# Kernel tuning notes

Measured on AMD Instinct MI355X. Metric: run time of the kernel, lower is better.

## Reference

```python
import jax, jax.numpy as jnp
import numpy as np

N_NODES, N_EDGES, NODE_D, EDGE_D, EMB_D, N_GRAPHS = 50000, 800000, 128, 100, 92, 256
N_CONV, FC_D, N_FC, CUTOFF = 3, 128, 2, 6.0


def setup_inputs() -> dict:
    key = jax.random.key(0)
    ks = jax.random.split(key, 24)
    s = 0.05
    inp = {
        "z": jax.random.randint(ks[0], (N_NODES,), 0, 100, dtype=jnp.int32),
        "R": jax.random.normal(ks[1], (N_NODES, 3), dtype=jnp.float32) * 5.0,
        "edge_index": jax.random.randint(ks[2], (2, N_EDGES), 0, N_NODES, dtype=jnp.int32),
        "batch": jnp.sort(jax.random.randint(ks[3], (N_NODES,), 0, N_GRAPHS, dtype=jnp.int32)),
        # learned parameters
        "embedding": jax.random.uniform(ks[4], (100, EMB_D), dtype=jnp.float32),
        "emb_w": jax.random.normal(ks[5], (EMB_D, NODE_D), dtype=jnp.float32) * s,
        "emb_b": jnp.zeros((NODE_D,), jnp.float32),
        "conv_w": jax.random.normal(ks[6], (N_CONV, 2 * NODE_D + EDGE_D, 2 * NODE_D), dtype=jnp.float32) * s,
        "conv_b": jnp.zeros((N_CONV, 2 * NODE_D), jnp.float32),
        "ln_g": jnp.ones((N_CONV, NODE_D), jnp.float32),
        "ln_b": jnp.zeros((N_CONV, NODE_D), jnp.float32),
        "cfc_w": jax.random.normal(ks[7], (NODE_D, FC_D), dtype=jnp.float32) * s,
        "cfc_b": jnp.zeros((FC_D,), jnp.float32),
        "fc_w": jax.random.normal(ks[8], (N_FC, FC_D, FC_D), dtype=jnp.float32) * s,
        "fc_b": jnp.zeros((N_FC, FC_D), jnp.float32),
        "out_w": jax.random.normal(ks[9], (FC_D, 1), dtype=jnp.float32) * s,
        "out_b": jnp.zeros((1,), jnp.float32),
    }
    return inp


def _gaussian_smearing(d):
    offsets = jnp.linspace(0.0, CUTOFF, EDGE_D, dtype=d.dtype)  # [EDGE_D]
    coeff = -0.5 / (offsets[1] - offsets[0]) ** 2
    return jnp.exp(coeff * (d[:, None] - offsets[None, :]) ** 2)  # [E, EDGE_D]


def _layernorm(x, g, b, eps=1e-5):
    mu = x.mean(-1, keepdims=True)
    var = x.var(-1, keepdims=True)
    return (x - mu) / jnp.sqrt(var + eps) * g + b


def reference(z, R, edge_index, batch, embedding, emb_w, emb_b, conv_w, conv_b,
              ln_g, ln_b, cfc_w, cfc_b, fc_w, fc_b, out_w, out_b):
    src, dst = edge_index[0], edge_index[1]  # messages flow src(j) -> dst(i)
    d = jnp.linalg.norm(R[src] - R[dst], axis=-1)  # [E]
    edge_attr = _gaussian_smearing(d)  # [E, EDGE_D]

    x = embedding[z] @ emb_w + emb_b  # [N, NODE_D]
    n = x.shape[0]
    for l in range(conv_w.shape[0]):
        xi, xj = x[dst], x[src]  # gather [E, NODE_D]
        zc = jnp.concatenate([xi, xj, edge_attr], axis=1) @ conv_w[l] + conv_b[l]  # [E, 2*NODE_D]
        z1, z2 = jnp.split(zc, 2, axis=1)
        msg = jax.nn.sigmoid(z1) * jax.nn.softplus(z2)  # [E, NODE_D]
        agg = jax.ops.segment_sum(msg, dst, num_segments=n)  # scatter-add
        x = jax.nn.softplus(_layernorm(agg, ln_g[l], ln_b[l]) + x)

    # global mean pool over graphs
    sums = jax.ops.segment_sum(x, batch, num_segments=N_GRAPHS)
    cnts = jax.ops.segment_sum(jnp.ones((n, 1), x.dtype), batch, num_segments=N_GRAPHS)
    mol = sums / jnp.maximum(cnts, 1.0)  # [N_GRAPHS, NODE_D]

    h = jax.nn.softplus(mol @ cfc_w + cfc_b)
    for l in range(fc_w.shape[0]):
        h = jax.nn.softplus(h @ fc_w[l] + fc_b[l])
    return h @ out_w + out_b  # energy [N_GRAPHS, 1]
```

## Files before the change

### kernel.cpp

```cpp
#include <hip/hip_runtime.h>
#include <hip/hip_bf16.h>
#include <cmath>

#define N_NODES 50000
#define N_EDGES 800000
#define NODE_DIM 128
#define EDGE_DIM 100
#define EMB_DIM 92
#define N_GRAPHS 256

typedef __attribute__((ext_vector_type(8))) short short8_t;
typedef __attribute__((ext_vector_type(4))) float float4_t;

__device__ __forceinline__ float softplus_f(float v) {
    return v > 20.0f ? v : __logf(1.0f + __expf(v));
}
__device__ __forceinline__ float sigmoid_f(float v) {
    return 1.0f / (1.0f + __expf(-v));
}

__global__ void deg_kernel(const int* __restrict__ ei, int* __restrict__ deg) {
    int e = blockIdx.x * blockDim.x + threadIdx.x;
    if (e >= N_EDGES) return;
    atomicAdd(&deg[ei[N_EDGES + e]], 1);
}

#define SB 1024
__global__ void scan1_kernel(const int* __restrict__ deg, int* __restrict__ rp,
                             int* __restrict__ bsum) {
    __shared__ int buf[SB];
    int b = blockIdx.x, t = threadIdx.x, i = b * SB + t;
    int v = (i < N_NODES) ? deg[i] : 0;
    buf[t] = v;
    __syncthreads();
    for (int off = 1; off < SB; off <<= 1) {
        int a = (t >= off) ? buf[t - off] : 0;
        __syncthreads();
        buf[t] += a;
        __syncthreads();
    }
    if (i < N_NODES) rp[i] = buf[t] - v;
    if (t == SB - 1) bsum[b] = buf[t];
}
__global__ void scan2_kernel(int* __restrict__ bsum, int n) {
    if (threadIdx.x == 0) {
        int s = 0;
        for (int i = 0; i < n; i++) { int v = bsum[i]; bsum[i] = s; s += v; }
    }
}
__global__ void scan3_kernel(int* __restrict__ rp, const int* __restrict__ bsum) {
    int i = blockIdx.x * SB + threadIdx.x;
    if (i < N_NODES) rp[i] += bsum[blockIdx.x];
    if (i == 0) rp[N_NODES] = N_EDGES;
}

__global__ void fill_kernel(const int* __restrict__ ei, const float* __restrict__ R,
                            const int* __restrict__ row_ptr, int* __restrict__ cnt2,
                            int* __restrict__ s_src, float* __restrict__ s_d) {
    int e = blockIdx.x * blockDim.x + threadIdx.x;
    if (e >= N_EDGES) return;
    int s = ei[e];
    int dst = ei[N_EDGES + e];
    float dx = R[3 * s + 0] - R[3 * dst + 0];
    float dy = R[3 * s + 1] - R[3 * dst + 1];
    float dz = R[3 * s + 2] - R[3 * dst + 2];
    float d = sqrtf(dx * dx + dy * dy + dz * dz);
    int pos = row_ptr[dst] + atomicAdd(&cnt2[dst], 1);
    s_src[pos] = s;
    s_d[pos] = d;
}

__global__ void gb_kernel(const int* __restrict__ batch, int* __restrict__ gs) {
    int i = blockIdx.x * 256 + threadIdx.x;
    if (i > N_NODES) return;
    int b = (i < N_NODES) ? batch[i] : N_GRAPHS;
    int pb = (i == 0) ? -1 : batch[i - 1];
    for (int g = pb + 1; g <= b; g++) gs[g] = i;
}

__global__ void wcvt_kernel(const float* __restrict__ conv_w, __hip_bfloat16* __restrict__ Webf) {
    int i = blockIdx.x * 256 + threadIdx.x;
    if (i >= 3 * EDGE_DIM * 256) return;
    int l = i / (EDGE_DIM * 256), r = i - l * (EDGE_DIM * 256);
    Webf[i] = (__hip_bfloat16)conv_w[(size_t)l * 356 * 256 + 256 * 256 + r];
}

__global__ void wprep_kernel(const float* __restrict__ conv_w, short* __restrict__ WbB) {
    int idx = blockIdx.x * 256 + threadIdx.x;
    if (idx >= 3 * 4 * 32 * 64 * 8) return;
    int j = idx & 7;
    int lane = (idx >> 3) & 63;
    int nt = (idx >> 9) & 31;
    int kc = (idx >> 14) & 3;
    int l = idx >> 16;
    int k = kc * 32 + (lane >> 4) * 8 + j;
    int nl = lane & 15;
    int row, col;
    if (nt < 16) { row = k; col = nt * 16 + nl; }
    else { row = 128 + k; col = (nt - 16) * 16 + nl; }
    __hip_bfloat16 bv = (__hip_bfloat16)conv_w[(size_t)l * 356 * 256 + (size_t)row * 256 + col];
    WbB[idx] = *(short*)&bv;
}

__global__ void embed_kernel(const int* __restrict__ z, const float* __restrict__ emb,
                             const float* __restrict__ emb_w, const float* __restrict__ emb_b,
                             float* __restrict__ x, __hip_bfloat16* __restrict__ xb) {
    __shared__ float er[EMB_DIM * 8];
    __shared__ int zi[8];
    int base = blockIdx.x * 8;
    int t = threadIdx.x;
    if (t < 8) zi[t] = z[base + t];
    __syncthreads();
    for (int idx = t; idx < EMB_DIM * 8; idx += 128) {
        int k = idx >> 3, j = idx & 7;
        er[idx] = emb[zi[j] * EMB_DIM + k];
    }
    __syncthreads();
    float acc[8];
    float bb = emb_b[t];
#pragma unroll
    for (int j = 0; j < 8; j++) acc[j] = bb;
    for (int k = 0; k < EMB_DIM; k++) {
        float w = emb_w[k * NODE_DIM + t];
        float4 ja = *(const float4*)&er[k * 8];
        float4 jb = *(const float4*)&er[k * 8 + 4];
        acc[0] = fmaf(w, ja.x, acc[0]); acc[1] = fmaf(w, ja.y, acc[1]);
        acc[2] = fmaf(w, ja.z, acc[2]); acc[3] = fmaf(w, ja.w, acc[3]);
        acc[4] = fmaf(w, jb.x, acc[4]); acc[5] = fmaf(w, jb.y, acc[5]);
        acc[6] = fmaf(w, jb.z, acc[6]); acc[7] = fmaf(w, jb.w, acc[7]);
    }
#pragma unroll
    for (int j = 0; j < 8; j++) {
        x[(base + j) * NODE_DIM + t] = acc[j];
        xb[(base + j) * NODE_DIM + t] = (__hip_bfloat16)acc[j];
    }
}

__global__ __launch_bounds__(256) void node_mfma_kernel(
    const __hip_bfloat16* __restrict__ xb, const short* __restrict__ WbB,
    const float* __restrict__ bl, float* __restrict__ P1, float* __restrict__ P2) {
    int t = threadIdx.x;
    int wv = t >> 6, lane = t & 63;
    int mrow = lane & 15, q = lane >> 4;
    int base = blockIdx.x * 16;
    const short* xr = (const short*)xb + (size_t)(base + mrow) * 128 + q * 8;
    float4_t acc[8];
#pragma unroll
    for (int i = 0; i < 8; i++) acc[i] = (float4_t){0.f, 0.f, 0.f, 0.f};
#pragma unroll
    for (int kc = 0; kc < 4; kc++) {
        short8_t a = *(const short8_t*)(xr + kc * 32);
#pragma unroll
        for (int i = 0; i < 8; i++) {
            int nt = wv * 8 + i;
            short8_t b = *(const short8_t*)&WbB[((size_t)(kc * 32 + nt) * 64 + lane) * 8];
            acc[i] = __builtin_amdgcn_mfma_f32_16x16x32_bf16(a, b, acc[i], 0, 0, 0);
        }
    }
#pragma unroll
    for (int i = 0; i < 8; i++) {
        int nt = wv * 8 + i;
        int np = nt * 16 + mrow;
        if (np < 256) {
            float bb = bl[np];
#pragma unroll
            for (int r = 0; r < 4; r++)
                P1[(size_t)(base + q * 4 + r) * 256 + np] = acc[i][r] + bb;
        } else {
#pragma unroll
            for (int r = 0; r < 4; r++)
                P2[(size_t)(base + q * 4 + r) * 256 + (np - 256)] = acc[i][r];
        }
    }
}

#define NTAP 10
__global__ __launch_bounds__(256) void node_edge_kernel(
    const int* __restrict__ row_ptr, const int* __restrict__ s_src,
    const float* __restrict__ s_d, const float* __restrict__ P1,
    const float* __restrict__ P2, const __hip_bfloat16* __restrict__ We,
    float* __restrict__ agg) {
    const float sp_ = 6.0f / 99.0f;
    const float inv_s = 99.0f / 6.0f;
    const float coeff = -0.5f * inv_s * inv_s;
    int node = blockIdx.x * 2 + (threadIdx.x >> 7);
    int c = threadIdx.x & 127;
    int e0 = row_ptr[node], e1 = row_ptr[node + 1];
    float a1 = P1[(size_t)node * 256 + c];
    float a2 = P1[(size_t)node * 256 + 128 + c];
    float acc = 0.f;
    float dvA = 0.f, b1A = 0.f, b2A = 0.f;
    int srcB = 0; float dvB = 0.f;
    if (e0 < e1) {
        int s0 = s_src[e0];
        dvA = s_d[e0];
        b1A = P2[(size_t)s0 * 256 + c];
        b2A = P2[(size_t)s0 * 256 + 128 + c];
    }
    if (e0 + 1 < e1) { srcB = s_src[e0 + 1]; dvB = s_d[e0 + 1]; }
    for (int e = e0; e < e1; e++) {
        float b1 = b1A, b2 = b2A, dv = dvA;
        if (e + 1 < e1) {
            b1A = P2[(size_t)srcB * 256 + c];
            b2A = P2[(size_t)srcB * 256 + 128 + c];
            dvA = dvB;
        }
        if (e + 2 < e1) { srcB = s_src[e + 2]; dvB = s_d[e + 2]; }
        float z1 = a1 + b1, z2 = a2 + b2;
        if (dv <= 6.34f) {
            int k0 = max(0, min(EDGE_DIM - NTAP, (int)ceilf(dv * inv_s - 4.5f)));
            const __hip_bfloat16* wr = We + k0 * 256 + c;
#pragma unroll
            for (int i = 0; i < NTAP; i++) {
                float df = dv - (float)(k0 + i) * sp_;
                float ee = __expf(coeff * df * df);
                z1 = fmaf((float)wr[i * 256], ee, z1);
                z2 = fmaf((float)wr[i * 256 + 128], ee, z2);
            }
        }
        acc += sigmoid_f(z1) * softplus_f(z2);
    }
    agg[(size_t)node * 128 + c] = acc;
}

__global__ void ln_kernel(const float* __restrict__ agg, const float* __restrict__ g,
                          const float* __restrict__ b, float* __restrict__ x,
                          __hip_bfloat16* __restrict__ xb) {
    __shared__ float sm[4][2];
    int t = threadIdx.x;
    int r = blockIdx.x * 2 + (t >> 7);
    int c = t & 127;
    float a = agg[(size_t)r * 128 + c];
    float s1 = a, s2 = a * a;
#pragma unroll
    for (int off = 32; off > 0; off >>= 1) {
        s1 += __shfl_xor(s1, off);
        s2 += __shfl_xor(s2, off);
    }
    int wv = t >> 6;
    if ((t & 63) == 0) { sm[wv][0] = s1; sm[wv][1] = s2; }
    __syncthreads();
    int w0 = (t >> 7) * 2;
    float S1 = sm[w0][0] + sm[w0 + 1][0];
    float S2 = sm[w0][1] + sm[w0 + 1][1];
    float mu = S1 * (1.0f / 128.0f);
    float var = S2 * (1.0f / 128.0f) - mu * mu;
    float rstd = rsqrtf(fmaxf(var, 0.f) + 1e-5f);
    float xv = x[(size_t)r * 128 + c];
    float res = softplus_f((a - mu) * rstd * g[c] + b[c] + xv);
    x[(size_t)r * 128 + c] = res;
    xb[(size_t)r * 128 + c] = (__hip_bfloat16)res;
}

__global__ void pool_head_kernel(const float* __restrict__ x, const int* __restrict__ gs,
                                 const float* __restrict__ cfc_w, const float* __restrict__ cfc_b,
                                 const float* __restrict__ fc_w, const float* __restrict__ fc_b,
                                 const float* __restrict__ out_w, const float* __restrict__ out_b,
                                 float* __restrict__ out) {
    int g = blockIdx.x, c = threadIdx.x;
    int n0 = gs[g], n1 = gs[g + 1];
    float s = 0.f;
    for (int n = n0; n < n1; n++) s += x[(size_t)n * 128 + c];
    __shared__ float h[128], h2[128];
    h[c] = s / fmaxf((float)(n1 - n0), 1.0f);
    __syncthreads();
    float acc = cfc_b[c];
    for (int k = 0; k < 128; k++) acc = fmaf(h[k], cfc_w[k * 128 + c], acc);
    h2[c] = softplus_f(acc);
    __syncthreads();
    for (int l = 0; l < 2; l++) {
        const float* W = fc_w + l * 128 * 128;
        acc = fc_b[l * 128 + c];
        for (int k = 0; k < 128; k++) acc = fmaf(h2[k], W[k * 128 + c], acc);
        __syncthreads();
        h2[c] = softplus_f(acc);
        __syncthreads();
    }
    h[c] = h2[c] * out_w[c];
    __syncthreads();
    for (int off = 64; off > 0; off >>= 1) {
        if (c < off) h[c] += h[c + off];
        __syncthreads();
    }
    if (c == 0) out[g] = h[0] + out_b[0];
}

extern "C" void kernel_launch(void* const* d_in, const int* in_sizes, int n_in,
                              void* d_out, int out_size, void* d_ws, size_t ws_size,
                              hipStream_t stream) {
    const int*   z      = (const int*)d_in[0];
    const float* R      = (const float*)d_in[1];
    const int*   ei     = (const int*)d_in[2];
    const int*   batch  = (const int*)d_in[3];
    const float* emb    = (const float*)d_in[4];
    const float* emb_w  = (const float*)d_in[5];
    const float* emb_b  = (const float*)d_in[6];
    const float* conv_w = (const float*)d_in[7];
    const float* conv_b = (const float*)d_in[8];
    const float* ln_g   = (const float*)d_in[9];
    const float* ln_b   = (const float*)d_in[10];
    const float* cfc_w  = (const float*)d_in[11];
    const float* cfc_b  = (const float*)d_in[12];
    const float* fc_w   = (const float*)d_in[13];
    const float* fc_b   = (const float*)d_in[14];
    const float* out_w  = (const float*)d_in[15];
    const float* out_b  = (const float*)d_in[16];
    float* out = (float*)d_out;

    float* ws    = (float*)d_ws;
    float* x     = ws;
    float* agg   = x + 6400000;
    float* P1    = agg + 6400000;
    float* P2    = P1 + 12800000;
    float* s_d   = P2 + 12800000;
    int* s_src   = (int*)(s_d + 800000);
    int* s_dst   = s_src + 800000;
    int* row_ptr = s_dst + 800000;
    int* deg     = row_ptr + 50004;
    int* cnt2    = deg + 50000;
    int* bsum    = cnt2 + 50000;
    int* gs      = bsum + 64;
    __hip_bfloat16* Webf = (__hip_bfloat16*)(gs + 260);
    short* WbB           = (short*)(Webf + 76800);
    __hip_bfloat16* xb   = (__hip_bfloat16*)(WbB + 196608);

    hipMemsetAsync(deg, 0, (size_t)100000 * 4, stream);
    deg_kernel<<<(N_EDGES + 255) / 256, 256, 0, stream>>>(ei, deg);
    int nsb = (N_NODES + SB - 1) / SB;
    scan1_kernel<<<nsb, SB, 0, stream>>>(deg, row_ptr, bsum);
    scan2_kernel<<<1, 64, 0, stream>>>(bsum, nsb);
    scan3_kernel<<<nsb, SB, 0, stream>>>(row_ptr, bsum);
    fill_kernel<<<(N_EDGES + 255) / 256, 256, 0, stream>>>(ei, R, row_ptr, cnt2,
                                                           s_src, s_d);
    gb_kernel<<<(N_NODES + 256) / 256 + 1, 256, 0, stream>>>(batch, gs);
    wcvt_kernel<<<(3 * EDGE_DIM * 256 + 255) / 256, 256, 0, stream>>>(conv_w, Webf);
    wprep_kernel<<<(3 * 4 * 32 * 64 * 8 + 255) / 256, 256, 0, stream>>>(conv_w, WbB);

    embed_kernel<<<N_NODES / 8, 128, 0, stream>>>(z, emb, emb_w, emb_b, x, xb);
    for (int l = 0; l < 3; l++) {
        node_mfma_kernel<<<N_NODES / 16, 256, 0, stream>>>(xb, WbB + (size_t)l * 65536,
                                                           conv_b + l * 256, P1, P2);
        node_edge_kernel<<<N_NODES / 2, 256, 0, stream>>>(row_ptr, s_src, s_d, P1, P2,
                                                          Webf + (size_t)l * EDGE_DIM * 256, agg);
        ln_kernel<<<N_NODES / 2, 256, 0, stream>>>(agg, ln_g + l * 128, ln_b + l * 128, x, xb);
    }
    pool_head_kernel<<<N_GRAPHS, 128, 0, stream>>>(x, gs, cfc_w, cfc_b, fc_w, fc_b,
                                                   out_w, out_b, out);
}
```

Before: 940.7 us.

## Fuse layernorm into edge aggregation kernel and deepen gather prefetch

Merges the layernorm/residual/softplus step into the edge message kernel, so the per-node aggregate stays in registers and never round-trips through global memory, and one launch per layer is dropped. The edge loop is also unrolled by two, with two-edge-deep prefetch of the P2 source rows and four-deep prefetch of edge indices and distances, to hide gather latency. The cost is higher register pressure from the extra in-flight loads, which could lower occupancy.

```diff
diff --git a/kernel.cpp b/kernel.cpp
--- a/kernel.cpp
+++ b/kernel.cpp
@@ -175,81 +175,100 @@
 }
 
 #define NTAP 10
-__global__ __launch_bounds__(256) void node_edge_kernel(
+__device__ __forceinline__ float edge_msg(float b1, float b2, float dv,
+                                          float a1, float a2,
+                                          const __hip_bfloat16* __restrict__ Wc) {
+    const float sp_ = 6.0f / 99.0f;
+    const float inv_s = 99.0f / 6.0f;
+    const float coeff = -0.5f * inv_s * inv_s;
+    float z1 = a1 + b1, z2 = a2 + b2;
+    if (dv <= 6.34f) {
+        int k0 = max(0, min(EDGE_DIM - NTAP, (int)ceilf(dv * inv_s - 4.5f)));
+        const __hip_bfloat16* wr = Wc + k0 * 256;
+#pragma unroll
+        for (int i = 0; i < NTAP; i++) {
+            float df = dv - (float)(k0 + i) * sp_;
+            float ee = __expf(coeff * df * df);
+            z1 = fmaf((float)wr[i * 256], ee, z1);
+            z2 = fmaf((float)wr[i * 256 + 128], ee, z2);
+        }
+    }
+    return sigmoid_f(z1) * softplus_f(z2);
+}
+
+__global__ __launch_bounds__(256) void node_edge_ln_kernel(
     const int* __restrict__ row_ptr, const int* __restrict__ s_src,
     const float* __restrict__ s_d, const float* __restrict__ P1,
     const float* __restrict__ P2, const __hip_bfloat16* __restrict__ We,
-    float* __restrict__ agg) {
-    const float sp_ = 6.0f / 99.0f;
-    const float inv_s = 99.0f / 6.0f;
-    const float coeff = -0.5f * inv_s * inv_s;
+    const float* __restrict__ lg, const float* __restrict__ lb,
+    float* __restrict__ x, __hip_bfloat16* __restrict__ xb) {
     int node = blockIdx.x * 2 + (threadIdx.x >> 7);
     int c = threadIdx.x & 127;
     int e0 = row_ptr[node], e1 = row_ptr[node + 1];
     float a1 = P1[(size_t)node * 256 + c];
     float a2 = P1[(size_t)node * 256 + 128 + c];
+    const __hip_bfloat16* Wc = We + c;
     float acc = 0.f;
-    float dvA = 0.f, b1A = 0.f, b2A = 0.f;
-    int srcB = 0; float dvB = 0.f;
+    float b1A = 0.f, b2A = 0.f, dvA = 0.f;
+    float b1B = 0.f, b2B = 0.f, dvB = 0.f;
+    int srcC = 0, srcD = 0;
+    float dC = 0.f, dD = 0.f;
     if (e0 < e1) {
-        int s0 = s_src[e0];
-        dvA = s_d[e0];
-        b1A = P2[(size_t)s0 * 256 + c];
-        b2A = P2[(size_t)s0 * 256 + 128 + c];
-    }
-    if (e0 + 1 < e1) { srcB = s_src[e0 + 1]; dvB = s_d[e0 + 1]; }
-    for (int e = e0; e < e1; e++) {
-        float b1 = b1A, b2 = b2A, dv = dvA;
-        if (e + 1 < e1) {
-            b1A = P2[(size_t)srcB * 256 + c];
-            b2A = P2[(size_t)srcB * 256 + 128 + c];
-            dvA = dvB;
-        }
-        if (e + 2 < e1) { srcB = s_src[e + 2]; dvB = s_d[e + 2]; }
-        float z1 = a1 + b1, z2 = a2 + b2;
-        if (dv <= 6.34f) {
-            int k0 = max(0, min(EDGE_DIM - NTAP, (int)ceilf(dv * inv_s - 4.5f)));
-            const __hip_bfloat16* wr = We + k0 * 256 + c;
-#pragma unroll
-            for (int i = 0; i < NTAP; i++) {
-                float df = dv - (float)(k0 + i) * sp_;
-                float ee = __expf(coeff * df * df);
-                z1 = fmaf((float)wr[i * 256], ee, z1);
-                z2 = fmaf((float)wr[i * 256 + 128], ee, z2);
+        int s = s_src[e0]; dvA = s_d[e0];
+        b1A = P2[(size_t)s * 256 + c]; b2A = P2[(size_t)s * 256 + 128 + c];
+    }
+    if (e0 + 1 < e1) {
+        int s = s_src[e0 + 1]; dvB = s_d[e0 + 1];
+        b1B = P2[(size_t)s * 256 + c]; b2B = P2[(size_t)s * 256 + 128 + c];
+    }
+    if (e0 + 2 < e1) { srcC = s_src[e0 + 2]; dC = s_d[e0 + 2]; }
+    if (e0 + 3 < e1) { srcD = s_src[e0 + 3]; dD = s_d[e0 + 3]; }
+    int e = e0;
+    while (e < e1) {
+        {
+            float b1 = b1A, b2 = b2A, dv = dvA;
+            if (e + 2 < e1) {
+                b1A = P2[(size_t)srcC * 256 + c];
+                b2A = P2[(size_t)srcC * 256 + 128 + c];
+                dvA = dC;
             }
-        }
-        acc += sigmoid_f(z1) * softplus_f(z2);
-    }
-    agg[(size_t)node * 128 + c] = acc;
-}
-
-__global__ void ln_kernel(const float* __restrict__ agg, const float* __restrict__ g,
-                          const float* __restrict__ b, float* __restrict__ x,
-                          __hip_bfloat16* __restrict__ xb) {
+            if (e + 4 < e1) { srcC = s_src[e + 4]; dC = s_d[e + 4]; }
+            acc += edge_msg(b1, b2, dv, a1, a2, Wc);
+        }
+        e++;
+        if (e >= e1) break;
+        {
+            float b1 = b1B, b2 = b2B, dv = dvB;
+            if (e + 2 < e1) {
+                b1B = P2[(size_t)srcD * 256 + c];
+                b2B = P2[(size_t)srcD * 256 + 128 + c];
+                dvB = dD;
+            }
+            if (e + 4 < e1) { srcD = s_src[e + 4]; dD = s_d[e + 4]; }
+            acc += edge_msg(b1, b2, dv, a1, a2, Wc);
+        }
+        e++;
+    }
     __shared__ float sm[4][2];
-    int t = threadIdx.x;
-    int r = blockIdx.x * 2 + (t >> 7);
-    int c = t & 127;
-    float a = agg[(size_t)r * 128 + c];
-    float s1 = a, s2 = a * a;
+    float s1 = acc, s2 = acc * acc;
 #pragma unroll
     for (int off = 32; off > 0; off >>= 1) {
         s1 += __shfl_xor(s1, off);
         s2 += __shfl_xor(s2, off);
     }
-    int wv = t >> 6;
-    if ((t & 63) == 0) { sm[wv][0] = s1; sm[wv][1] = s2; }
-    __syncthreads();
-    int w0 = (t >> 7) * 2;
+    int wv = threadIdx.x >> 6;
+    if ((threadIdx.x & 63) == 0) { sm[wv][0] = s1; sm[wv][1] = s2; }
+    __syncthreads();
+    int w0 = (threadIdx.x >> 7) * 2;
     float S1 = sm[w0][0] + sm[w0 + 1][0];
     float S2 = sm[w0][1] + sm[w0 + 1][1];
     float mu = S1 * (1.0f / 128.0f);
     float var = S2 * (1.0f / 128.0f) - mu * mu;
     float rstd = rsqrtf(fmaxf(var, 0.f) + 1e-5f);
-    float xv = x[(size_t)r * 128 + c];
-    float res = softplus_f((a - mu) * rstd * g[c] + b[c] + xv);
-    x[(size_t)r * 128 + c] = res;
-    xb[(size_t)r * 128 + c] = (__hip_bfloat16)res;
+    float xv = x[(size_t)node * 128 + c];
+    float res = softplus_f((acc - mu) * rstd * lg[c] + lb[c] + xv);
+    x[(size_t)node * 128 + c] = res;
+    xb[(size_t)node * 128 + c] = (__hip_bfloat16)res;
 }
 
 __global__ void pool_head_kernel(const float* __restrict__ x, const int* __restrict__ gs,
@@ -340,9 +359,9 @@
     for (int l = 0; l < 3; l++) {
         node_mfma_kernel<<<N_NODES / 16, 256, 0, stream>>>(xb, WbB + (size_t)l * 65536,
                                                            conv_b + l * 256, P1, P2);
-        node_edge_kernel<<<N_NODES / 2, 256, 0, stream>>>(row_ptr, s_src, s_d, P1, P2,
-                                                          Webf + (size_t)l * EDGE_DIM * 256, agg);
-        ln_kernel<<<N_NODES / 2, 256, 0, stream>>>(agg, ln_g + l * 128, ln_b + l * 128, x, xb);
+        node_edge_ln_kernel<<<N_NODES / 2, 256, 0, stream>>>(
+            row_ptr, s_src, s_d, P1, P2, Webf + (size_t)l * EDGE_DIM * 256,
+            ln_g + l * 128, ln_b + l * 128, x, xb);
     }
     pool_head_kernel<<<N_GRAPHS, 128, 0, stream>>>(x, gs, cfc_w, cfc_b, fc_w, fc_b,
                                                    out_w, out_b, out);
```

Measured after the change: 914.0 us. 2.8% less time.
